# Optimization experiments

Hardware: AMD Instinct MI355X
Metric: run time of the kernel (lower is better)

The kernel has to match this reference:

```python
import jax, jax.numpy as jnp
import numpy as np

N, D, OUT, K = 100000, 256, 128, 10
N1, B = 40960, 4096


def setup_inputs() -> dict:
    key = jax.random.key(0)
    k1, k2, k3, k4, k5, k6, k7 = jax.random.split(key, 7)
    raw_features = jax.random.normal(k1, (N, D), dtype=jnp.float32)
    # xavier-ish init for SageLayer weights [out, 2*in]
    W1 = jax.random.normal(k2, (OUT, 2 * D), dtype=jnp.float32) * (2.0 / (OUT + 2 * D)) ** 0.5
    W2 = jax.random.normal(k3, (OUT, 2 * OUT), dtype=jnp.float32) * (2.0 / (OUT + 2 * OUT)) ** 0.5
    nodes1 = jax.random.randint(k4, (N1,), 0, N)              # layer-1 node ids into raw table
    neighs1 = jax.random.randint(k5, (N1, K), 0, N)           # sampled neighbors (ids into raw table)
    map2 = jax.random.randint(k6, (B,), 0, N1)                # self-index of batch nodes into layer-1 rows
    neighs2 = jax.random.randint(k7, (B, K), 0, N1)           # sampled neighbors (rows of layer-1 embs)
    return {"raw_features": raw_features, "W1": W1, "W2": W2,
            "nodes1": nodes1, "neighs1": neighs1, "map2": map2, "neighs2": neighs2}


def reference(raw_features, W1, W2, nodes1, neighs1, map2, neighs2):
    # Layer 1: mean-aggregate sampled neighbor features (= mask.div(num_neigh).mm(embed_matrix))
    agg1 = jnp.mean(raw_features[neighs1], axis=1)                      # [N1, D]
    self1 = raw_features[nodes1]                                        # [N1, D]
    h1 = jax.nn.relu(jnp.concatenate([self1, agg1], axis=1) @ W1.T)     # [N1, OUT]
    # Layer 2
    agg2 = jnp.mean(h1[neighs2], axis=1)                                # [B, OUT]
    self2 = h1[map2]                                                    # [B, OUT]
    h2 = jax.nn.relu(jnp.concatenate([self2, agg2], axis=1) @ W2.T)     # [B, OUT]
    return h2
```

## Files before the change

### kernel.cpp

```cpp
#include <hip/hip_runtime.h>
#include <hip/hip_bf16.h>

#define N_RAW  100000
#define DIM    256
#define OUTD   128
#define KN     10
#define N1N    40960
#define BATCH  4096

typedef __attribute__((ext_vector_type(8))) short bf16x8;
typedef __attribute__((ext_vector_type(4))) float f32x4;
typedef unsigned int u32;

static __device__ inline float b2f(short s) {
  unsigned u = ((unsigned)(unsigned short)s) << 16;
  return __builtin_bit_cast(float, u);
}
static __device__ inline short f2b(float f) {
  unsigned u = __builtin_bit_cast(unsigned, f);
  unsigned r = (u + 0x7fff + ((u >> 16) & 1)) >> 16;
  return (short)r;
}

static __device__ inline void gload_lds16(const void* g, void* l) {
  __builtin_amdgcn_global_load_lds((const __attribute__((address_space(1))) u32*)g,
                                   (__attribute__((address_space(3))) u32*)l, 16, 0, 0);
}

__global__ void build_wc(const float* __restrict__ W1, const float* __restrict__ W2,
                         short* __restrict__ W1c, short* __restrict__ W2c) {
  int i = blockIdx.x * blockDim.x + threadIdx.x;
  {
    int j = i >> 8, k = i & 255;
    float v = (j < OUTD) ? W1[j * (2 * DIM) + k] : W1[(j - OUTD) * (2 * DIM) + DIM + k];
    u32 byte = (u32)(j * 512 + k * 2) ^ ((u32)(j & 7) << 4);
    *(short*)((char*)W1c + byte) = f2b(v);
  }
  if (i < 256 * 128) {
    int j = i >> 7, k = i & 127;
    float v = (j < OUTD) ? W2[j * (2 * OUTD) + k] : W2[(j - OUTD) * (2 * OUTD) + OUTD + k];
    u32 byte = (u32)(j * 256 + k * 2) ^ ((u32)(j & 7) << 4);
    *(short*)((char*)W2c + byte) = f2b(v);
  }
}

__launch_bounds__(512, 2)
__global__ void gemm_P(const float* __restrict__ raw, const short* __restrict__ W1c,
                       short* __restrict__ P) {
  __shared__ short Wlds[256 * 256];
  const int tid  = threadIdx.x;
  const int wave = tid >> 6, lane = tid & 63;
  const int r16  = lane & 15, kg = lane >> 4;
  const int m0   = blockIdx.x * 128 + wave * 16;

  int arow = m0 + r16; if (arow >= N_RAW) arow = N_RAW - 1;
  const float* xrow = raw + (size_t)arow * DIM + kg * 8;
  float4 af[16];
#pragma unroll
  for (int ks = 0; ks < 8; ++ks) {
    af[2 * ks]     = *(const float4*)(xrow + ks * 32);
    af[2 * ks + 1] = *(const float4*)(xrow + ks * 32 + 4);
  }

#pragma unroll
  for (int it = 0; it < 16; ++it)
    gload_lds16((const char*)W1c + it * 8192 + tid * 16,
                (char*)Wlds + it * 8192 + wave * 1024);
  __syncthreads();

  bf16x8 ab[8];
#pragma unroll
  for (int ks = 0; ks < 8; ++ks) {
    bf16x8 t;
    t[0] = f2b(af[2 * ks].x);     t[1] = f2b(af[2 * ks].y);
    t[2] = f2b(af[2 * ks].z);     t[3] = f2b(af[2 * ks].w);
    t[4] = f2b(af[2 * ks + 1].x); t[5] = f2b(af[2 * ks + 1].y);
    t[6] = f2b(af[2 * ks + 1].z); t[7] = f2b(af[2 * ks + 1].w);
    ab[ks] = t;
  }

  f32x4 acc[16];
#pragma unroll
  for (int n = 0; n < 16; ++n) acc[n] = (f32x4){0.f, 0.f, 0.f, 0.f};

#pragma unroll
  for (int ks = 0; ks < 8; ++ks) {
#pragma unroll
    for (int n = 0; n < 16; ++n) {
      u32 byte = (u32)((n * 16 + r16) * 512 + ks * 64 + kg * 16) ^ ((u32)(r16 & 7) << 4);
      bf16x8 b = *(const bf16x8*)((const char*)Wlds + byte);
      acc[n] = __builtin_amdgcn_mfma_f32_16x16x32_bf16(ab[ks], b, acc[n], 0, 0, 0);
    }
  }

#pragma unroll
  for (int n = 0; n < 16; ++n)
#pragma unroll
    for (int j = 0; j < 4; ++j) {
      int r = m0 + kg * 4 + j;
      if (r < N_RAW) P[(size_t)r * 256 + (n * 16 + r16)] = f2b(acc[n][j]);
    }
}

__launch_bounds__(512, 4)
__global__ void gemm_Q(const short* __restrict__ h1, const short* __restrict__ W2c,
                       short* __restrict__ Q) {
  __shared__ short Wlds[256 * 128];
  const int tid  = threadIdx.x;
  const int wave = tid >> 6, lane = tid & 63;
  const int r16  = lane & 15, kg = lane >> 4;
  const int m0   = blockIdx.x * 128 + wave * 16;

  const short* xrow = h1 + (size_t)(m0 + r16) * OUTD + kg * 8;
  bf16x8 ab[4];
#pragma unroll
  for (int ks = 0; ks < 4; ++ks) ab[ks] = *(const bf16x8*)(xrow + ks * 32);

#pragma unroll
  for (int it = 0; it < 8; ++it)
    gload_lds16((const char*)W2c + it * 8192 + tid * 16,
                (char*)Wlds + it * 8192 + wave * 1024);
  __syncthreads();

  f32x4 acc[16];
#pragma unroll
  for (int n = 0; n < 16; ++n) acc[n] = (f32x4){0.f, 0.f, 0.f, 0.f};

#pragma unroll
  for (int ks = 0; ks < 4; ++ks) {
#pragma unroll
    for (int n = 0; n < 16; ++n) {
      u32 byte = (u32)((n * 16 + r16) * 256 + ks * 64 + kg * 16) ^ ((u32)(r16 & 7) << 4);
      bf16x8 b = *(const bf16x8*)((const char*)Wlds + byte);
      acc[n] = __builtin_amdgcn_mfma_f32_16x16x32_bf16(ab[ks], b, acc[n], 0, 0, 0);
    }
  }

#pragma unroll
  for (int n = 0; n < 16; ++n)
#pragma unroll
    for (int j = 0; j < 4; ++j)
      Q[(size_t)(m0 + kg * 4 + j) * 256 + (n * 16 + r16)] = f2b(acc[n][j]);
}

__global__ void gather1(const short* __restrict__ P, const int* __restrict__ nodes1,
                        const int* __restrict__ neighs1, short* __restrict__ h1) {
  int g = threadIdx.x >> 4, t = threadIdx.x & 15;
  int row = blockIdx.x * 16 + g;
  int sn = nodes1[row];
  bf16x8 sv = *(const bf16x8*)(P + (size_t)sn * 256 + t * 8);
  float acc[8];
#pragma unroll
  for (int e = 0; e < 8; ++e) acc[e] = 0.f;
#pragma unroll
  for (int k = 0; k < KN; ++k) {
    int nn = neighs1[row * KN + k];
    bf16x8 nv = *(const bf16x8*)(P + (size_t)nn * 256 + 128 + t * 8);
#pragma unroll
    for (int e = 0; e < 8; ++e) acc[e] += b2f(nv[e]);
  }
  bf16x8 o;
#pragma unroll
  for (int e = 0; e < 8; ++e) o[e] = f2b(fmaxf(b2f(sv[e]) + 0.1f * acc[e], 0.f));
  *(bf16x8*)(h1 + (size_t)row * OUTD + t * 8) = o;
}

__global__ void gather2(const short* __restrict__ Q, const int* __restrict__ map2,
                        const int* __restrict__ neighs2, float* __restrict__ out) {
  int g = threadIdx.x >> 4, t = threadIdx.x & 15;
  int row = blockIdx.x * 16 + g;
  int sn = map2[row];
  bf16x8 sv = *(const bf16x8*)(Q + (size_t)sn * 256 + t * 8);
  float acc[8];
#pragma unroll
  for (int e = 0; e < 8; ++e) acc[e] = 0.f;
#pragma unroll
  for (int k = 0; k < KN; ++k) {
    int nn = neighs2[row * KN + k];
    bf16x8 nv = *(const bf16x8*)(Q + (size_t)nn * 256 + 128 + t * 8);
#pragma unroll
    for (int e = 0; e < 8; ++e) acc[e] += b2f(nv[e]);
  }
  float* orow = out + (size_t)row * OUTD + t * 8;
  float4 o0, o1;
  o0.x = fmaxf(b2f(sv[0]) + 0.1f * acc[0], 0.f);
  o0.y = fmaxf(b2f(sv[1]) + 0.1f * acc[1], 0.f);
  o0.z = fmaxf(b2f(sv[2]) + 0.1f * acc[2], 0.f);
  o0.w = fmaxf(b2f(sv[3]) + 0.1f * acc[3], 0.f);
  o1.x = fmaxf(b2f(sv[4]) + 0.1f * acc[4], 0.f);
  o1.y = fmaxf(b2f(sv[5]) + 0.1f * acc[5], 0.f);
  o1.z = fmaxf(b2f(sv[6]) + 0.1f * acc[6], 0.f);
  o1.w = fmaxf(b2f(sv[7]) + 0.1f * acc[7], 0.f);
  *(float4*)orow = o0;
  *(float4*)(orow + 4) = o1;
}

extern "C" void kernel_launch(void* const* d_in, const int* in_sizes, int n_in,
                              void* d_out, int out_size, void* d_ws, size_t ws_size,
                              hipStream_t stream) {
  const float* raw     = (const float*)d_in[0];
  const float* W1      = (const float*)d_in[1];
  const float* W2      = (const float*)d_in[2];
  const int*   nodes1  = (const int*)d_in[3];
  const int*   neighs1 = (const int*)d_in[4];
  const int*   map2    = (const int*)d_in[5];
  const int*   neighs2 = (const int*)d_in[6];
  float* out = (float*)d_out;

  char* ws = (char*)d_ws;
  short* W1c = (short*)(ws);
  short* W2c = (short*)(ws + 131072);
  short* P   = (short*)(ws + 196608);
  short* Q   = (short*)(ws + 196608);
  short* h1  = (short*)(ws + 51396608);

  build_wc<<<256, 256, 0, stream>>>(W1, W2, W1c, W2c);
  gemm_P<<<782, 512, 0, stream>>>(raw, W1c, P);
  gather1<<<N1N / 16, 256, 0, stream>>>(P, nodes1, neighs1, h1);
  gemm_Q<<<N1N / 128, 512, 0, stream>>>(h1, W2c, Q);
  gather2<<<BATCH / 16, 256, 0, stream>>>(Q, map2, neighs2, out);
}
```

Baseline: 93.22 us.

## Split gemm_P K into halves with 64KB LDS and 32-row waves

Reorganizes the weight buffer into two K-halves so gemm_P stages only 64KB of weights in LDS at a time. Blocks shrink to 4 waves, and each wave handles 32 rows, so each B fragment read from LDS feeds two MFMAs. The second half of the raw rows is loaded while the first half is being multiplied. This halves LDS use per block to allow more resident blocks and cuts LDS reads per MFMA, at the cost of an extra barrier phase and a weight reload into LDS.

Result: no change. 91.54 us (-1.8%).

```diff
diff --git a/kernel.cpp b/kernel.cpp
--- a/kernel.cpp
+++ b/kernel.cpp
@@ -33,7 +33,8 @@
   {
     int j = i >> 8, k = i & 255;
     float v = (j < OUTD) ? W1[j * (2 * DIM) + k] : W1[(j - OUTD) * (2 * DIM) + DIM + k];
-    u32 byte = (u32)(j * 512 + k * 2) ^ ((u32)(j & 7) << 4);
+    int h = k >> 7, kk = k & 127;
+    u32 byte = (u32)(h * 65536) + (((u32)(j * 256 + kk * 2)) ^ ((u32)(j & 7) << 4));
     *(short*)((char*)W1c + byte) = f2b(v);
   }
   if (i < 256 * 128) {
@@ -44,62 +45,111 @@
   }
 }
 
-__launch_bounds__(512, 2)
+__launch_bounds__(256, 2)
 __global__ void gemm_P(const float* __restrict__ raw, const short* __restrict__ W1c,
                        short* __restrict__ P) {
-  __shared__ short Wlds[256 * 256];
+  __shared__ short Bh[256 * 128];
   const int tid  = threadIdx.x;
   const int wave = tid >> 6, lane = tid & 63;
   const int r16  = lane & 15, kg = lane >> 4;
-  const int m0   = blockIdx.x * 128 + wave * 16;
-
-  int arow = m0 + r16; if (arow >= N_RAW) arow = N_RAW - 1;
-  const float* xrow = raw + (size_t)arow * DIM + kg * 8;
+  const int m0   = blockIdx.x * 128 + wave * 32;
+
+  int r0 = m0 + r16;      if (r0 > N_RAW - 1) r0 = N_RAW - 1;
+  int r1 = m0 + 16 + r16; if (r1 > N_RAW - 1) r1 = N_RAW - 1;
+  const float* x0 = raw + (size_t)r0 * DIM + kg * 8;
+  const float* x1 = raw + (size_t)r1 * DIM + kg * 8;
+
   float4 af[16];
 #pragma unroll
-  for (int ks = 0; ks < 8; ++ks) {
-    af[2 * ks]     = *(const float4*)(xrow + ks * 32);
-    af[2 * ks + 1] = *(const float4*)(xrow + ks * 32 + 4);
+  for (int ks = 0; ks < 4; ++ks) {
+    af[ks * 2]         = *(const float4*)(x0 + ks * 32);
+    af[ks * 2 + 1]     = *(const float4*)(x0 + ks * 32 + 4);
+    af[8 + ks * 2]     = *(const float4*)(x1 + ks * 32);
+    af[8 + ks * 2 + 1] = *(const float4*)(x1 + ks * 32 + 4);
   }
 
 #pragma unroll
   for (int it = 0; it < 16; ++it)
-    gload_lds16((const char*)W1c + it * 8192 + tid * 16,
-                (char*)Wlds + it * 8192 + wave * 1024);
-  __syncthreads();
-
-  bf16x8 ab[8];
-#pragma unroll
-  for (int ks = 0; ks < 8; ++ks) {
-    bf16x8 t;
-    t[0] = f2b(af[2 * ks].x);     t[1] = f2b(af[2 * ks].y);
-    t[2] = f2b(af[2 * ks].z);     t[3] = f2b(af[2 * ks].w);
-    t[4] = f2b(af[2 * ks + 1].x); t[5] = f2b(af[2 * ks + 1].y);
-    t[6] = f2b(af[2 * ks + 1].z); t[7] = f2b(af[2 * ks + 1].w);
-    ab[ks] = t;
-  }
-
-  f32x4 acc[16];
-#pragma unroll
-  for (int n = 0; n < 16; ++n) acc[n] = (f32x4){0.f, 0.f, 0.f, 0.f};
-
-#pragma unroll
-  for (int ks = 0; ks < 8; ++ks) {
+    gload_lds16((const char*)W1c + it * 4096 + tid * 16,
+                (char*)Bh + it * 4096 + wave * 1024);
+
+  bf16x8 a0[2][4];
+#pragma unroll
+  for (int s = 0; s < 2; ++s)
+#pragma unroll
+    for (int ks = 0; ks < 4; ++ks) {
+      float4 lo = af[s * 8 + ks * 2], hi = af[s * 8 + ks * 2 + 1];
+      bf16x8 t;
+      t[0] = f2b(lo.x); t[1] = f2b(lo.y); t[2] = f2b(lo.z); t[3] = f2b(lo.w);
+      t[4] = f2b(hi.x); t[5] = f2b(hi.y); t[6] = f2b(hi.z); t[7] = f2b(hi.w);
+      a0[s][ks] = t;
+    }
+
+  f32x4 acc[2][16];
+#pragma unroll
+  for (int s = 0; s < 2; ++s)
+#pragma unroll
+    for (int n = 0; n < 16; ++n) acc[s][n] = (f32x4){0.f, 0.f, 0.f, 0.f};
+
+  __syncthreads();
+
+#pragma unroll
+  for (int ks = 0; ks < 4; ++ks) {
+    af[ks * 2]         = *(const float4*)(x0 + 128 + ks * 32);
+    af[ks * 2 + 1]     = *(const float4*)(x0 + 128 + ks * 32 + 4);
+    af[8 + ks * 2]     = *(const float4*)(x1 + 128 + ks * 32);
+    af[8 + ks * 2 + 1] = *(const float4*)(x1 + 128 + ks * 32 + 4);
+  }
+
+#pragma unroll
+  for (int ks = 0; ks < 4; ++ks)
 #pragma unroll
     for (int n = 0; n < 16; ++n) {
-      u32 byte = (u32)((n * 16 + r16) * 512 + ks * 64 + kg * 16) ^ ((u32)(r16 & 7) << 4);
-      bf16x8 b = *(const bf16x8*)((const char*)Wlds + byte);
-      acc[n] = __builtin_amdgcn_mfma_f32_16x16x32_bf16(ab[ks], b, acc[n], 0, 0, 0);
-    }
-  }
-
-#pragma unroll
-  for (int n = 0; n < 16; ++n)
-#pragma unroll
-    for (int j = 0; j < 4; ++j) {
-      int r = m0 + kg * 4 + j;
-      if (r < N_RAW) P[(size_t)r * 256 + (n * 16 + r16)] = f2b(acc[n][j]);
-    }
+      u32 byte = (u32)((n * 16 + r16) * 256 + ks * 64 + kg * 16) ^ ((u32)(r16 & 7) << 4);
+      bf16x8 b = *(const bf16x8*)((const char*)Bh + byte);
+      acc[0][n] = __builtin_amdgcn_mfma_f32_16x16x32_bf16(a0[0][ks], b, acc[0][n], 0, 0, 0);
+      acc[1][n] = __builtin_amdgcn_mfma_f32_16x16x32_bf16(a0[1][ks], b, acc[1][n], 0, 0, 0);
+    }
+
+  __syncthreads();
+
+#pragma unroll
+  for (int it = 0; it < 16; ++it)
+    gload_lds16((const char*)W1c + 65536 + it * 4096 + tid * 16,
+                (char*)Bh + it * 4096 + wave * 1024);
+
+#pragma unroll
+  for (int s = 0; s < 2; ++s)
+#pragma unroll
+    for (int ks = 0; ks < 4; ++ks) {
+      float4 lo = af[s * 8 + ks * 2], hi = af[s * 8 + ks * 2 + 1];
+      bf16x8 t;
+      t[0] = f2b(lo.x); t[1] = f2b(lo.y); t[2] = f2b(lo.z); t[3] = f2b(lo.w);
+      t[4] = f2b(hi.x); t[5] = f2b(hi.y); t[6] = f2b(hi.z); t[7] = f2b(hi.w);
+      a0[s][ks] = t;
+    }
+
+  __syncthreads();
+
+#pragma unroll
+  for (int ks = 0; ks < 4; ++ks)
+#pragma unroll
+    for (int n = 0; n < 16; ++n) {
+      u32 byte = (u32)((n * 16 + r16) * 256 + ks * 64 + kg * 16) ^ ((u32)(r16 & 7) << 4);
+      bf16x8 b = *(const bf16x8*)((const char*)Bh + byte);
+      acc[0][n] = __builtin_amdgcn_mfma_f32_16x16x32_bf16(a0[0][ks], b, acc[0][n], 0, 0, 0);
+      acc[1][n] = __builtin_amdgcn_mfma_f32_16x16x32_bf16(a0[1][ks], b, acc[1][n], 0, 0, 0);
+    }
+
+#pragma unroll
+  for (int s = 0; s < 2; ++s)
+#pragma unroll
+    for (int n = 0; n < 16; ++n)
+#pragma unroll
+      for (int j = 0; j < 4; ++j) {
+        int r = m0 + s * 16 + kg * 4 + j;
+        if (r < N_RAW) P[(size_t)r * 256 + (n * 16 + r16)] = f2b(acc[s][n][j]);
+      }
 }
 
 __launch_bounds__(512, 4)
@@ -215,7 +265,7 @@
   short* h1  = (short*)(ws + 51396608);
 
   build_wc<<<256, 256, 0, stream>>>(W1, W2, W1c, W2c);
-  gemm_P<<<782, 512, 0, stream>>>(raw, W1c, P);
+  gemm_P<<<782, 256, 0, stream>>>(raw, W1c, P);
   gather1<<<N1N / 16, 256, 0, stream>>>(P, nodes1, neighs1, h1);
   gemm_Q<<<N1N / 128, 512, 0, stream>>>(h1, W2c, Q);
   gather2<<<BATCH / 16, 256, 0, stream>>>(Q, map2, neighs2, out);
```

## Hold weights in registers and use persistent grid-stride GEMMs with prefetch

Applied to the files above, without the earlier changes.

Both GEMMs drop the LDS weight staging. Each wave now keeps its 64-column slice of the weight matrix in registers, and a persistent grid of blocks loops over 16-row strips, prefetching the next strip's inputs while the current MFMAs run. This removes the per-block reload of the full weight tile into LDS, the LDS reads and the barrier, in exchange for heavy register pressure. Every row strip is now read by four waves instead of one, so redundant input traffic relies on cache hits, and occupancy drops.

New measurement: 111.9 us. 20.0% more time.

```diff
diff --git a/kernel.cpp b/kernel.cpp
--- a/kernel.cpp
+++ b/kernel.cpp
@@ -8,6 +8,11 @@
 #define N1N    40960
 #define BATCH  4096
 
+#define SNP    6252
+#define NBP    512
+#define SNQ    2560
+#define NBQ    256
+
 typedef __attribute__((ext_vector_type(8))) short bf16x8;
 typedef __attribute__((ext_vector_type(4))) float f32x4;
 typedef unsigned int u32;
@@ -20,11 +25,6 @@
   unsigned u = __builtin_bit_cast(unsigned, f);
   unsigned r = (u + 0x7fff + ((u >> 16) & 1)) >> 16;
   return (short)r;
-}
-
-static __device__ inline void gload_lds16(const void* g, void* l) {
-  __builtin_amdgcn_global_load_lds((const __attribute__((address_space(1))) u32*)g,
-                                   (__attribute__((address_space(3))) u32*)l, 16, 0, 0);
 }
 
 __global__ void build_wc(const float* __restrict__ W1, const float* __restrict__ W2,
@@ -33,114 +33,134 @@
   {
     int j = i >> 8, k = i & 255;
     float v = (j < OUTD) ? W1[j * (2 * DIM) + k] : W1[(j - OUTD) * (2 * DIM) + DIM + k];
-    u32 byte = (u32)(j * 512 + k * 2) ^ ((u32)(j & 7) << 4);
-    *(short*)((char*)W1c + byte) = f2b(v);
+    W1c[j * 256 + k] = f2b(v);
   }
   if (i < 256 * 128) {
     int j = i >> 7, k = i & 127;
     float v = (j < OUTD) ? W2[j * (2 * OUTD) + k] : W2[(j - OUTD) * (2 * OUTD) + OUTD + k];
-    u32 byte = (u32)(j * 256 + k * 2) ^ ((u32)(j & 7) << 4);
-    *(short*)((char*)W2c + byte) = f2b(v);
-  }
-}
-
-__launch_bounds__(512, 2)
+    W2c[j * 128 + k] = f2b(v);
+  }
+}
+
+__launch_bounds__(256, 2)
 __global__ void gemm_P(const float* __restrict__ raw, const short* __restrict__ W1c,
                        short* __restrict__ P) {
-  __shared__ short Wlds[256 * 256];
   const int tid  = threadIdx.x;
   const int wave = tid >> 6, lane = tid & 63;
   const int r16  = lane & 15, kg = lane >> 4;
-  const int m0   = blockIdx.x * 128 + wave * 16;
-
-  int arow = m0 + r16; if (arow >= N_RAW) arow = N_RAW - 1;
-  const float* xrow = raw + (size_t)arow * DIM + kg * 8;
+  const int col0 = wave * 64;
+
+  bf16x8 B[4][8];
+#pragma unroll
+  for (int n = 0; n < 4; ++n)
+#pragma unroll
+    for (int ks = 0; ks < 8; ++ks)
+      B[n][ks] = *(const bf16x8*)(W1c + (size_t)(col0 + n * 16 + r16) * 256 + ks * 32 + kg * 8);
+
+  int s = blockIdx.x;
   float4 af[16];
-#pragma unroll
-  for (int ks = 0; ks < 8; ++ks) {
-    af[2 * ks]     = *(const float4*)(xrow + ks * 32);
-    af[2 * ks + 1] = *(const float4*)(xrow + ks * 32 + 4);
-  }
-
-#pragma unroll
-  for (int it = 0; it < 16; ++it)
-    gload_lds16((const char*)W1c + it * 8192 + tid * 16,
-                (char*)Wlds + it * 8192 + wave * 1024);
-  __syncthreads();
-
-  bf16x8 ab[8];
-#pragma unroll
-  for (int ks = 0; ks < 8; ++ks) {
-    bf16x8 t;
-    t[0] = f2b(af[2 * ks].x);     t[1] = f2b(af[2 * ks].y);
-    t[2] = f2b(af[2 * ks].z);     t[3] = f2b(af[2 * ks].w);
-    t[4] = f2b(af[2 * ks + 1].x); t[5] = f2b(af[2 * ks + 1].y);
-    t[6] = f2b(af[2 * ks + 1].z); t[7] = f2b(af[2 * ks + 1].w);
-    ab[ks] = t;
-  }
-
-  f32x4 acc[16];
-#pragma unroll
-  for (int n = 0; n < 16; ++n) acc[n] = (f32x4){0.f, 0.f, 0.f, 0.f};
-
-#pragma unroll
-  for (int ks = 0; ks < 8; ++ks) {
-#pragma unroll
-    for (int n = 0; n < 16; ++n) {
-      u32 byte = (u32)((n * 16 + r16) * 512 + ks * 64 + kg * 16) ^ ((u32)(r16 & 7) << 4);
-      bf16x8 b = *(const bf16x8*)((const char*)Wlds + byte);
-      acc[n] = __builtin_amdgcn_mfma_f32_16x16x32_bf16(ab[ks], b, acc[n], 0, 0, 0);
-    }
-  }
-
-#pragma unroll
-  for (int n = 0; n < 16; ++n)
-#pragma unroll
-    for (int j = 0; j < 4; ++j) {
-      int r = m0 + kg * 4 + j;
-      if (r < N_RAW) P[(size_t)r * 256 + (n * 16 + r16)] = f2b(acc[n][j]);
-    }
-}
-
-__launch_bounds__(512, 4)
+  {
+    int r = s * 16 + r16; if (r > N_RAW - 1) r = N_RAW - 1;
+    const float* x = raw + (size_t)r * DIM + kg * 8;
+#pragma unroll
+    for (int ks = 0; ks < 8; ++ks) {
+      af[2 * ks]     = *(const float4*)(x + ks * 32);
+      af[2 * ks + 1] = *(const float4*)(x + ks * 32 + 4);
+    }
+  }
+
+  for (; s < SNP; s += NBP) {
+    bf16x8 ab[8];
+#pragma unroll
+    for (int ks = 0; ks < 8; ++ks) {
+      float4 lo = af[2 * ks], hi = af[2 * ks + 1];
+      bf16x8 t;
+      t[0] = f2b(lo.x); t[1] = f2b(lo.y); t[2] = f2b(lo.z); t[3] = f2b(lo.w);
+      t[4] = f2b(hi.x); t[5] = f2b(hi.y); t[6] = f2b(hi.z); t[7] = f2b(hi.w);
+      ab[ks] = t;
+    }
+    {
+      int sn = s + NBP; if (sn >= SNP) sn = s;
+      int r = sn * 16 + r16; if (r > N_RAW - 1) r = N_RAW - 1;
+      const float* x = raw + (size_t)r * DIM + kg * 8;
+#pragma unroll
+      for (int ks = 0; ks < 8; ++ks) {
+        af[2 * ks]     = *(const float4*)(x + ks * 32);
+        af[2 * ks + 1] = *(const float4*)(x + ks * 32 + 4);
+      }
+    }
+
+    f32x4 acc[4];
+#pragma unroll
+    for (int n = 0; n < 4; ++n) acc[n] = (f32x4){0.f, 0.f, 0.f, 0.f};
+#pragma unroll
+    for (int ks = 0; ks < 8; ++ks)
+#pragma unroll
+      for (int n = 0; n < 4; ++n)
+        acc[n] = __builtin_amdgcn_mfma_f32_16x16x32_bf16(ab[ks], B[n][ks], acc[n], 0, 0, 0);
+
+    int rbase = s * 16 + kg * 4;
+#pragma unroll
+    for (int n = 0; n < 4; ++n)
+#pragma unroll
+      for (int j = 0; j < 4; ++j) {
+        int r = rbase + j;
+        if (r < N_RAW) P[(size_t)r * 256 + (col0 + n * 16 + r16)] = f2b(acc[n][j]);
+      }
+  }
+}
+
+__launch_bounds__(256, 3)
 __global__ void gemm_Q(const short* __restrict__ h1, const short* __restrict__ W2c,
                        short* __restrict__ Q) {
-  __shared__ short Wlds[256 * 128];
   const int tid  = threadIdx.x;
   const int wave = tid >> 6, lane = tid & 63;
   const int r16  = lane & 15, kg = lane >> 4;
-  const int m0   = blockIdx.x * 128 + wave * 16;
-
-  const short* xrow = h1 + (size_t)(m0 + r16) * OUTD + kg * 8;
-  bf16x8 ab[4];
-#pragma unroll
-  for (int ks = 0; ks < 4; ++ks) ab[ks] = *(const bf16x8*)(xrow + ks * 32);
-
-#pragma unroll
-  for (int it = 0; it < 8; ++it)
-    gload_lds16((const char*)W2c + it * 8192 + tid * 16,
-                (char*)Wlds + it * 8192 + wave * 1024);
-  __syncthreads();
-
-  f32x4 acc[16];
-#pragma unroll
-  for (int n = 0; n < 16; ++n) acc[n] = (f32x4){0.f, 0.f, 0.f, 0.f};
-
-#pragma unroll
-  for (int ks = 0; ks < 4; ++ks) {
-#pragma unroll
-    for (int n = 0; n < 16; ++n) {
-      u32 byte = (u32)((n * 16 + r16) * 256 + ks * 64 + kg * 16) ^ ((u32)(r16 & 7) << 4);
-      bf16x8 b = *(const bf16x8*)((const char*)Wlds + byte);
-      acc[n] = __builtin_amdgcn_mfma_f32_16x16x32_bf16(ab[ks], b, acc[n], 0, 0, 0);
-    }
-  }
-
-#pragma unroll
-  for (int n = 0; n < 16; ++n)
-#pragma unroll
-    for (int j = 0; j < 4; ++j)
-      Q[(size_t)(m0 + kg * 4 + j) * 256 + (n * 16 + r16)] = f2b(acc[n][j]);
+  const int col0 = wave * 64;
+
+  bf16x8 B[4][4];
+#pragma unroll
+  for (int n = 0; n < 4; ++n)
+#pragma unroll
+    for (int ks = 0; ks < 4; ++ks)
+      B[n][ks] = *(const bf16x8*)(W2c + (size_t)(col0 + n * 16 + r16) * 128 + ks * 32 + kg * 8);
+
+  int s = blockIdx.x;
+  bf16x8 acur[4];
+  {
+    const short* x = h1 + (size_t)(s * 16 + r16) * OUTD + kg * 8;
+#pragma unroll
+    for (int ks = 0; ks < 4; ++ks) acur[ks] = *(const bf16x8*)(x + ks * 32);
+  }
+
+  for (; s < SNQ; s += NBQ) {
+    bf16x8 anxt[4];
+    {
+      int sn = s + NBQ; if (sn >= SNQ) sn = s;
+      const short* x = h1 + (size_t)(sn * 16 + r16) * OUTD + kg * 8;
+#pragma unroll
+      for (int ks = 0; ks < 4; ++ks) anxt[ks] = *(const bf16x8*)(x + ks * 32);
+    }
+
+    f32x4 acc[4];
+#pragma unroll
+    for (int n = 0; n < 4; ++n) acc[n] = (f32x4){0.f, 0.f, 0.f, 0.f};
+#pragma unroll
+    for (int ks = 0; ks < 4; ++ks)
+#pragma unroll
+      for (int n = 0; n < 4; ++n)
+        acc[n] = __builtin_amdgcn_mfma_f32_16x16x32_bf16(acur[ks], B[n][ks], acc[n], 0, 0, 0);
+
+    int rbase = s * 16 + kg * 4;
+#pragma unroll
+    for (int n = 0; n < 4; ++n)
+#pragma unroll
+      for (int j = 0; j < 4; ++j)
+        Q[(size_t)(rbase + j) * 256 + (col0 + n * 16 + r16)] = f2b(acc[n][j]);
+
+#pragma unroll
+    for (int ks = 0; ks < 4; ++ks) acur[ks] = anxt[ks];
+  }
 }
 
 __global__ void gather1(const short* __restrict__ P, const int* __restrict__ nodes1,
@@ -215,8 +235,8 @@
   short* h1  = (short*)(ws + 51396608);
 
   build_wc<<<256, 256, 0, stream>>>(W1, W2, W1c, W2c);
-  gemm_P<<<782, 512, 0, stream>>>(raw, W1c, P);
+  gemm_P<<<NBP, 256, 0, stream>>>(raw, W1c, P);
   gather1<<<N1N / 16, 256, 0, stream>>>(P, nodes1, neighs1, h1);
-  gemm_Q<<<N1N / 128, 512, 0, stream>>>(h1, W2c, Q);
+  gemm_Q<<<NBQ, 256, 0, stream>>>(h1, W2c, Q);
   gather2<<<BATCH / 16, 256, 0, stream>>>(Q, map2, neighs2, out);
 }
```

## Retile gemm_P into K-looped 128x128 LDS tiles with packed bf16 conversion

Applied to the files above, without the earlier changes.

Restructures the raw-feature GEMM. Each block now computes a 128x128 output tile (half the output columns) with a 4-step K loop. A and B 64-wide K slices are staged in 32KB of LDS, and W1c is re-laid out into per-slice swizzled blocks. Each wave computes a 64x64 sub-tile, so fragments are reused across both rows and columns. The fp32-to-bf16 conversion uses the packed v_cvt_pk_bf16_f32 instruction. This replaces the 128KB full-weight LDS staging to cut LDS footprint and raise occupancy, at the cost of reading raw features twice (once per column half) and adding per-step barriers without double buffering.

New measurement: 94.09 us. Within noise of the previous version (+0.9%).

```diff
diff --git a/kernel.cpp b/kernel.cpp
--- a/kernel.cpp
+++ b/kernel.cpp
@@ -21,7 +21,11 @@
   unsigned r = (u + 0x7fff + ((u >> 16) & 1)) >> 16;
   return (short)r;
 }
-
+static __device__ inline u32 cvtpk(float lo, float hi) {
+  u32 r;
+  asm("v_cvt_pk_bf16_f32 %0, %1, %2" : "=v"(r) : "v"(lo), "v"(hi));
+  return r;
+}
 static __device__ inline void gload_lds16(const void* g, void* l) {
   __builtin_amdgcn_global_load_lds((const __attribute__((address_space(1))) u32*)g,
                                    (__attribute__((address_space(3))) u32*)l, 16, 0, 0);
@@ -33,7 +37,9 @@
   {
     int j = i >> 8, k = i & 255;
     float v = (j < OUTD) ? W1[j * (2 * DIM) + k] : W1[(j - OUTD) * (2 * DIM) + DIM + k];
-    u32 byte = (u32)(j * 512 + k * 2) ^ ((u32)(j & 7) << 4);
+    int c = j >> 7, kk = k >> 6;
+    u32 byte = (u32)((c * 4 + kk) * 16384)
+             + ((((u32)(j & 127)) * 128 + ((u32)(k & 63)) * 2) ^ ((u32)(j & 7) << 4));
     *(short*)((char*)W1c + byte) = f2b(v);
   }
   if (i < 256 * 128) {
@@ -44,62 +50,94 @@
   }
 }
 
-__launch_bounds__(512, 2)
+__launch_bounds__(256, 3)
 __global__ void gemm_P(const float* __restrict__ raw, const short* __restrict__ W1c,
                        short* __restrict__ P) {
-  __shared__ short Wlds[256 * 256];
+  __shared__ char lds[32768];
+  char* Ab = lds;
+  char* Bb = lds + 16384;
+
   const int tid  = threadIdx.x;
   const int wave = tid >> 6, lane = tid & 63;
   const int r16  = lane & 15, kg = lane >> 4;
-  const int m0   = blockIdx.x * 128 + wave * 16;
-
-  int arow = m0 + r16; if (arow >= N_RAW) arow = N_RAW - 1;
-  const float* xrow = raw + (size_t)arow * DIM + kg * 8;
-  float4 af[16];
-#pragma unroll
-  for (int ks = 0; ks < 8; ++ks) {
-    af[2 * ks]     = *(const float4*)(xrow + ks * 32);
-    af[2 * ks + 1] = *(const float4*)(xrow + ks * 32 + 4);
-  }
-
-#pragma unroll
-  for (int it = 0; it < 16; ++it)
-    gload_lds16((const char*)W1c + it * 8192 + tid * 16,
-                (char*)Wlds + it * 8192 + wave * 1024);
-  __syncthreads();
-
-  bf16x8 ab[8];
-#pragma unroll
-  for (int ks = 0; ks < 8; ++ks) {
-    bf16x8 t;
-    t[0] = f2b(af[2 * ks].x);     t[1] = f2b(af[2 * ks].y);
-    t[2] = f2b(af[2 * ks].z);     t[3] = f2b(af[2 * ks].w);
-    t[4] = f2b(af[2 * ks + 1].x); t[5] = f2b(af[2 * ks + 1].y);
-    t[6] = f2b(af[2 * ks + 1].z); t[7] = f2b(af[2 * ks + 1].w);
-    ab[ks] = t;
-  }
-
-  f32x4 acc[16];
-#pragma unroll
-  for (int n = 0; n < 16; ++n) acc[n] = (f32x4){0.f, 0.f, 0.f, 0.f};
-
-#pragma unroll
-  for (int ks = 0; ks < 8; ++ks) {
-#pragma unroll
-    for (int n = 0; n < 16; ++n) {
-      u32 byte = (u32)((n * 16 + r16) * 512 + ks * 64 + kg * 16) ^ ((u32)(r16 & 7) << 4);
-      bf16x8 b = *(const bf16x8*)((const char*)Wlds + byte);
-      acc[n] = __builtin_amdgcn_mfma_f32_16x16x32_bf16(ab[ks], b, acc[n], 0, 0, 0);
+  const int wr   = wave >> 1, wc = wave & 1;
+  const int c    = blockIdx.x & 1;
+  const int m0   = (blockIdx.x >> 1) * 128;
+  const u32 swz  = (u32)(r16 & 7) << 4;
+
+  const int srow = tid >> 1, shalf = tid & 1;
+  int grow = m0 + srow; if (grow > N_RAW - 1) grow = N_RAW - 1;
+  const float* gA = raw + (size_t)grow * DIM + shalf * 32;
+  const u32 wswz = (u32)(srow & 7) << 4;
+  char* aw = Ab + (u32)(srow * 128);
+
+  f32x4 acc[4][4];
+#pragma unroll
+  for (int mi = 0; mi < 4; ++mi)
+#pragma unroll
+    for (int n = 0; n < 4; ++n) acc[mi][n] = (f32x4){0.f, 0.f, 0.f, 0.f};
+
+  const char* Wt = (const char*)W1c + c * 4 * 16384;
+
+  for (int kk = 0; kk < 4; ++kk) {
+#pragma unroll
+    for (int j = 0; j < 4; ++j)
+      gload_lds16(Wt + kk * 16384 + j * 4096 + wave * 1024 + lane * 16,
+                  Bb + j * 4096 + wave * 1024);
+    {
+      const float* g = gA + kk * 64;
+      float4 v[8];
+#pragma unroll
+      for (int i = 0; i < 8; ++i) v[i] = *(const float4*)(g + i * 4);
+      u32 w[16];
+#pragma unroll
+      for (int i = 0; i < 8; ++i) {
+        w[2 * i]     = cvtpk(v[i].x, v[i].y);
+        w[2 * i + 1] = cvtpk(v[i].z, v[i].w);
+      }
+#pragma unroll
+      for (int j = 0; j < 4; ++j) {
+        uint4 q; q.x = w[4 * j]; q.y = w[4 * j + 1]; q.z = w[4 * j + 2]; q.w = w[4 * j + 3];
+        *(uint4*)(aw + (((u32)(shalf * 64 + j * 16)) ^ wswz)) = q;
+      }
     }
-  }
-
-#pragma unroll
-  for (int n = 0; n < 16; ++n)
-#pragma unroll
-    for (int j = 0; j < 4; ++j) {
-      int r = m0 + kg * 4 + j;
-      if (r < N_RAW) P[(size_t)r * 256 + (n * 16 + r16)] = f2b(acc[n][j]);
+    __syncthreads();
+
+    bf16x8 a[4][2], b[4][2];
+#pragma unroll
+    for (int ks = 0; ks < 2; ++ks) {
+#pragma unroll
+      for (int mi = 0; mi < 4; ++mi) {
+        u32 byte = ((u32)((wr * 64 + mi * 16 + r16) * 128 + ks * 64 + kg * 16)) ^ swz;
+        a[mi][ks] = *(const bf16x8*)(Ab + byte);
+      }
+#pragma unroll
+      for (int n = 0; n < 4; ++n) {
+        u32 byte = ((u32)((wc * 64 + n * 16 + r16) * 128 + ks * 64 + kg * 16)) ^ swz;
+        b[n][ks] = *(const bf16x8*)(Bb + byte);
+      }
     }
+#pragma unroll
+    for (int ks = 0; ks < 2; ++ks)
+#pragma unroll
+      for (int mi = 0; mi < 4; ++mi)
+#pragma unroll
+        for (int n = 0; n < 4; ++n)
+          acc[mi][n] = __builtin_amdgcn_mfma_f32_16x16x32_bf16(a[mi][ks], b[n][ks], acc[mi][n], 0, 0, 0);
+
+    if (kk < 3) __syncthreads();
+  }
+
+#pragma unroll
+  for (int mi = 0; mi < 4; ++mi)
+#pragma unroll
+    for (int n = 0; n < 4; ++n)
+#pragma unroll
+      for (int j = 0; j < 4; ++j) {
+        int r = m0 + wr * 64 + mi * 16 + kg * 4 + j;
+        if (r < N_RAW)
+          P[(size_t)r * 256 + (c * 128 + wc * 64 + n * 16 + r16)] = f2b(acc[mi][n][j]);
+      }
 }
 
 __launch_bounds__(512, 4)
@@ -215,7 +253,7 @@
   short* h1  = (short*)(ws + 51396608);
 
   build_wc<<<256, 256, 0, stream>>>(W1, W2, W1c, W2c);
-  gemm_P<<<782, 512, 0, stream>>>(raw, W1c, P);
+  gemm_P<<<1564, 256, 0, stream>>>(raw, W1c, P);
   gather1<<<N1N / 16, 256, 0, stream>>>(P, nodes1, neighs1, h1);
   gemm_Q<<<N1N / 128, 512, 0, stream>>>(h1, W2c, Q);
   gather2<<<BATCH / 16, 256, 0, stream>>>(Q, map2, neighs2, out);
```
